# Kernel tuning notes

Hardware: AMD Instinct MI355X
Metric: run time of the kernel (lower is better)

The kernel has to match this reference:

```python
import jax, jax.numpy as jnp
import numpy as np

N, IN_DIM, HID = 8192, 128, 64
LEAKY_SLOPE = 0.2
MASK_VAL = -9e15


def lstm_step(x, W_ih, W_hh, b_ih, b_hh, h0, c0):
    # PyTorch LSTM single time step, gate order i, f, g, o
    gates = x @ W_ih.T + b_ih + h0 @ W_hh.T + b_hh
    i, f, g, o = jnp.split(gates, 4, axis=-1)
    c = jax.nn.sigmoid(f) * c0 + jax.nn.sigmoid(i) * jnp.tanh(g)
    h = jax.nn.sigmoid(o) * jnp.tanh(c)
    return h, c


def setup_inputs() -> dict:
    key = jax.random.key(0)
    ks = jax.random.split(key, 10)
    sc = 0.05
    x = jax.random.normal(ks[0], (N, IN_DIM), jnp.float32)
    adj = jax.random.randint(ks[1], (N, N), 0, 2).astype(jnp.float32)
    fea_W = jax.random.normal(ks[2], (IN_DIM, HID), jnp.float32) * sc
    fea_b = jnp.zeros((HID,), jnp.float32)
    gat_W = jax.random.normal(ks[3], (HID, IN_DIM), jnp.float32) * sc
    gat_a = jax.random.normal(ks[4], (2 * IN_DIM,), jnp.float32) * sc
    enc_W_ih = jax.random.normal(ks[5], (4 * HID, IN_DIM), jnp.float32) * sc
    enc_W_hh = jax.random.normal(ks[6], (4 * HID, HID), jnp.float32) * sc
    enc_b_ih = jnp.zeros((4 * HID,), jnp.float32)
    enc_b_hh = jnp.zeros((4 * HID,), jnp.float32)
    dec_W_ih = jax.random.normal(ks[7], (4 * IN_DIM, HID), jnp.float32) * sc
    dec_W_hh = jax.random.normal(ks[8], (4 * IN_DIM, IN_DIM), jnp.float32) * sc
    dec_b_ih = jnp.zeros((4 * IN_DIM,), jnp.float32)
    dec_b_hh = jnp.zeros((4 * IN_DIM,), jnp.float32)
    return dict(x=x, adj=adj, fea_W=fea_W, fea_b=fea_b, gat_W=gat_W, gat_a=gat_a,
                enc_W_ih=enc_W_ih, enc_W_hh=enc_W_hh, enc_b_ih=enc_b_ih, enc_b_hh=enc_b_hh,
                dec_W_ih=dec_W_ih, dec_W_hh=dec_W_hh, dec_b_ih=dec_b_ih, dec_b_hh=dec_b_hh)


def reference(x, adj, fea_W, fea_b, gat_W, gat_a,
              enc_W_ih, enc_W_hh, enc_b_ih, enc_b_hh,
              dec_W_ih, dec_W_hh, dec_b_ih, dec_b_hh):
    # structure branch: Linear + ReLU then GAT layer
    structure = jax.nn.relu(x @ fea_W + fea_b)            # [N, HID]
    Wh = structure @ gat_W                                # [N, IN_DIM]
    a1, a2 = gat_a[:IN_DIM], gat_a[IN_DIM:]
    e = jax.nn.leaky_relu((Wh @ a1)[:, None] + (Wh @ a2)[None, :], LEAKY_SLOPE)  # [N, N]
    scores = jnp.where(adj > 0, e, MASK_VAL)
    att = jax.nn.softmax(scores, axis=1)
    emb = jax.nn.elu(att @ Wh)                            # [N, IN_DIM]
    # attribute branch: seq_len=1 encoder/decoder LSTM with zero init states
    h0e = jnp.zeros((N, HID), x.dtype)
    h_enc, _ = lstm_step(x, enc_W_ih, enc_W_hh, enc_b_ih, enc_b_hh, h0e, h0e)
    h0d = jnp.zeros((N, IN_DIM), x.dtype)
    att_adj, _ = lstm_step(h_enc, dec_W_ih, dec_W_hh, dec_b_ih, dec_b_hh, h0d, h0d)  # [N, IN_DIM]
    con_adj = emb @ emb.T                                 # [N, N]
    return con_adj, att_adj
```

## Files before the change

### kernel.cpp

```cpp
#include <hip/hip_runtime.h>
#include <hip/hip_bf16.h>

typedef __hip_bfloat16 bf16_t;
typedef short bf16x8 __attribute__((ext_vector_type(8)));
typedef float f32x4 __attribute__((ext_vector_type(4)));

#define NROW 8192
#define LEAKY 0.2f

__device__ __forceinline__ float b2f(bf16_t v){ return __bfloat162float(v); }
__device__ __forceinline__ unsigned short f2b(float f){
  union { bf16_t h; unsigned short u; } cv; cv.h = __float2bfloat16(f); return cv.u;
}
__device__ __forceinline__ float sigf(float v){ return 1.0f / (1.0f + __expf(-v)); }

__global__ void k_probe(const unsigned short* __restrict__ x_raw, int* __restrict__ flag)
{
  const int lane = threadIdx.x;
  int cnt = 0;
  for (int k = lane; k < 512; k += 64){
    const int e = (x_raw[k] >> 7) & 0xff;
    cnt += (e >= 120 && e <= 130) ? 1 : 0;
  }
  #pragma unroll
  for (int s = 1; s < 64; s <<= 1) cnt += __shfl_xor(cnt, s, 64);
  if (lane == 0) flag[0] = (cnt < 384) ? 1 : 0;
}

__global__ __launch_bounds__(256) void k_cvt(
    const void* __restrict__ encW, const void* __restrict__ decW,
    const int* __restrict__ flag,
    unsigned short* __restrict__ encWb, unsigned short* __restrict__ decWb)
{
  const int idx = blockIdx.x*256 + threadIdx.x;
  const int isf32 = flag[0];
  if (idx < 32768){
    float v = isf32 ? ((const float*)encW)[idx] : b2f(((const bf16_t*)encW)[idx]);
    encWb[idx] = f2b(v);
  } else {
    const int j = idx - 32768;
    float v = isf32 ? ((const float*)decW)[j] : b2f(((const bf16_t*)decW)[j]);
    decWb[j] = f2b(v);
  }
}

__global__ __launch_bounds__(256) void k_feamask(
    const void* __restrict__ x, const void* __restrict__ adj,
    const void* __restrict__ fea_W, const void* __restrict__ fea_b,
    const void* __restrict__ gat_W, const void* __restrict__ gat_a,
    const int* __restrict__ flag,
    unsigned short* __restrict__ Whb_p, float* __restrict__ s1, float* __restrict__ s2,
    unsigned short* __restrict__ xb, unsigned char* __restrict__ mask8)
{
  const int r = blockIdx.x, tid = threadIdx.x;
  const int isf32 = flag[0];

  float4 mv0, mv1, mv2, mv3, mv4, mv5, mv6, mv7;
  bf16x8 bv0, bv1, bv2, bv3;
  if (isf32){
    const float4* arow = (const float4*)((const float*)adj + (size_t)r*NROW);
    mv0 = arow[(size_t)tid*2];         mv1 = arow[(size_t)tid*2+1];
    mv2 = arow[(size_t)(tid+256)*2];   mv3 = arow[(size_t)(tid+256)*2+1];
    mv4 = arow[(size_t)(tid+512)*2];   mv5 = arow[(size_t)(tid+512)*2+1];
    mv6 = arow[(size_t)(tid+768)*2];   mv7 = arow[(size_t)(tid+768)*2+1];
  } else {
    const unsigned short* arow = (const unsigned short*)adj + (size_t)r*NROW;
    bv0 = *(const bf16x8*)(arow + (size_t)tid*8);
    bv1 = *(const bf16x8*)(arow + (size_t)(tid+256)*8);
    bv2 = *(const bf16x8*)(arow + (size_t)(tid+512)*8);
    bv3 = *(const bf16x8*)(arow + (size_t)(tid+768)*8);
  }

  if (tid < 64){
    const int l = tid;
    float x0, x1;
    if (isf32){
      const float* xr = (const float*)x + (size_t)r*128;
      x0 = xr[l]; x1 = xr[l+64];
    } else {
      const bf16_t* xr = (const bf16_t*)x + (size_t)r*128;
      x0 = b2f(xr[l]); x1 = b2f(xr[l+64]);
    }
    xb[(size_t)r*128 + l]      = f2b(x0);
    xb[(size_t)r*128 + 64 + l] = f2b(x1);

    float acc = isf32 ? ((const float*)fea_b)[l] : b2f(((const bf16_t*)fea_b)[l]);
    if (isf32){
      const float* W = (const float*)fea_W;
      #pragma unroll
      for (int d=0; d<64; ++d) acc = fmaf(__shfl(x0, d, 64), W[d*64+l], acc);
      #pragma unroll
      for (int d=0; d<64; ++d) acc = fmaf(__shfl(x1, d, 64), W[(d+64)*64+l], acc);
    } else {
      const bf16_t* W = (const bf16_t*)fea_W;
      #pragma unroll
      for (int d=0; d<64; ++d) acc = fmaf(__shfl(x0, d, 64), b2f(W[d*64+l]), acc);
      #pragma unroll
      for (int d=0; d<64; ++d) acc = fmaf(__shfl(x1, d, 64), b2f(W[(d+64)*64+l]), acc);
    }
    const float stv = fmaxf(acc, 0.0f);

    float w0 = 0.f, w1 = 0.f;
    if (isf32){
      const float* W = (const float*)gat_W;
      #pragma unroll
      for (int d=0; d<64; ++d){
        const float sd = __shfl(stv, d, 64);
        w0 = fmaf(sd, W[d*128+l],    w0);
        w1 = fmaf(sd, W[d*128+64+l], w1);
      }
    } else {
      const bf16_t* W = (const bf16_t*)gat_W;
      #pragma unroll
      for (int d=0; d<64; ++d){
        const float sd = __shfl(stv, d, 64);
        w0 = fmaf(sd, b2f(W[d*128+l]),    w0);
        w1 = fmaf(sd, b2f(W[d*128+64+l]), w1);
      }
    }

    const size_t pbase = (size_t)(r >> 3)*1024 + (r & 7);
    Whb_p[pbase + (size_t)l*8]      = f2b(w0);
    Whb_p[pbase + (size_t)(l+64)*8] = f2b(w1);

    float a10, a11, a20, a21;
    if (isf32){
      const float* A = (const float*)gat_a;
      a10 = A[l]; a11 = A[l+64]; a20 = A[128+l]; a21 = A[192+l];
    } else {
      const bf16_t* A = (const bf16_t*)gat_a;
      a10 = b2f(A[l]); a11 = b2f(A[l+64]); a20 = b2f(A[128+l]); a21 = b2f(A[192+l]);
    }
    float r1 = w0*a10 + w1*a11;
    float r2 = w0*a20 + w1*a21;
    #pragma unroll
    for (int s=1; s<64; s<<=1){ r1 += __shfl_xor(r1, s, 64); r2 += __shfl_xor(r2, s, 64); }
    if (l == 0){ s1[r] = r1; s2[r] = r2; }
  }

  if (isf32){
    const float4 va[8] = { mv0, mv1, mv2, mv3, mv4, mv5, mv6, mv7 };
    #pragma unroll
    for (int k=0;k<4;++k){
      const float4 v0 = va[2*k], v1 = va[2*k+1];
      unsigned int m =
          (unsigned int)(v0.x>0.f)      | ((unsigned int)(v0.y>0.f)<<1) |
          ((unsigned int)(v0.z>0.f)<<2) | ((unsigned int)(v0.w>0.f)<<3) |
          ((unsigned int)(v1.x>0.f)<<4) | ((unsigned int)(v1.y>0.f)<<5) |
          ((unsigned int)(v1.z>0.f)<<6) | ((unsigned int)(v1.w>0.f)<<7);
      mask8[(size_t)r*1024 + tid + k*256] = (unsigned char)m;
    }
  } else {
    const bf16x8 vb[4] = { bv0, bv1, bv2, bv3 };
    #pragma unroll
    for (int k=0;k<4;++k){
      unsigned int m = 0;
      #pragma unroll
      for (int j=0;j<8;++j){
        union { short s; unsigned short u; } cv; cv.s = vb[k][j];
        union { unsigned short u; bf16_t h; } cv2; cv2.u = cv.u;
        m |= ((unsigned int)(b2f(cv2.h) > 0.f)) << j;
      }
      mask8[(size_t)r*1024 + tid + k*256] = (unsigned char)m;
    }
  }
}

__global__ __launch_bounds__(256) void k_enc2(
    const unsigned short* __restrict__ xb, const unsigned short* __restrict__ Wb,
    const void* __restrict__ b_ih, const void* __restrict__ b_hh,
    const int* __restrict__ flag, unsigned short* __restrict__ h_enc_b)
{
  __shared__ float g_lds[32][257];
  const int tid = threadIdx.x, lane = tid & 63, wv = tid >> 6;
  const int quad = lane >> 4, nn = lane & 15;
  const int rowbase = blockIdx.x * 32;
  const int rows_off = (wv & 1) * 16;
  const int col_off  = (wv >> 1) * 128;

  f32x4 acc[8];
  #pragma unroll
  for (int t=0;t<8;++t) acc[t] = (f32x4){0.f,0.f,0.f,0.f};

  #pragma unroll
  for (int ks=0; ks<4; ++ks){
    const int kb = ks*32 + quad*8;
    bf16x8 afrag = *(const bf16x8*)(xb + (size_t)(rowbase + rows_off + nn)*128 + kb);
    #pragma unroll
    for (int t=0;t<8;++t){
      bf16x8 bfrag = *(const bf16x8*)(Wb + (size_t)(col_off + t*16 + nn)*128 + kb);
      acc[t] = __builtin_amdgcn_mfma_f32_16x16x32_bf16(afrag, bfrag, acc[t], 0, 0, 0);
    }
  }
  #pragma unroll
  for (int t=0;t<8;++t)
    #pragma unroll
    for (int r=0;r<4;++r)
      g_lds[rows_off + quad*4 + r][col_off + t*16 + nn] = acc[t][r];
  __syncthreads();

  const int isf32 = flag[0];
  #pragma unroll
  for (int k=0;k<8;++k){
    const int idx = tid + k*256;
    const int r = idx >> 6, hid = idx & 63;
    float bi, bg, bo;
    if (isf32){
      const float* bi1 = (const float*)b_ih; const float* bi2 = (const float*)b_hh;
      bi = bi1[hid]     + bi2[hid];
      bg = bi1[128+hid] + bi2[128+hid];
      bo = bi1[192+hid] + bi2[192+hid];
    } else {
      const bf16_t* bi1 = (const bf16_t*)b_ih; const bf16_t* bi2 = (const bf16_t*)b_hh;
      bi = b2f(bi1[hid])     + b2f(bi2[hid]);
      bg = b2f(bi1[128+hid]) + b2f(bi2[128+hid]);
      bo = b2f(bi1[192+hid]) + b2f(bi2[192+hid]);
    }
    const float gi = g_lds[r][hid]     + bi;
    const float gg = g_lds[r][128+hid] + bg;
    const float go = g_lds[r][192+hid] + bo;
    const float c = tanhf(gg) * sigf(gi);
    const float h = tanhf(c)  * sigf(go);
    h_enc_b[(size_t)(rowbase + r)*64 + hid] = f2b(h);
  }
}

__global__ __launch_bounds__(256) void k_dec2(
    const unsigned short* __restrict__ hb, const unsigned short* __restrict__ Wb,
    const void* __restrict__ b_ih, const void* __restrict__ b_hh,
    const int* __restrict__ flag, void* __restrict__ d_out)
{
  __shared__ float g_lds[16][517];
  const int tid = threadIdx.x, lane = tid & 63, wv = tid >> 6;
  const int quad = lane >> 4, nn = lane & 15;
  const int rowbase = blockIdx.x * 16;
  const int col_off = wv * 128;

  f32x4 acc[8];
  #pragma unroll
  for (int t=0;t<8;++t) acc[t] = (f32x4){0.f,0.f,0.f,0.f};

  #pragma unroll
  for (int ks=0; ks<2; ++ks){
    const int kb = ks*32 + quad*8;
    bf16x8 afrag = *(const bf16x8*)(hb + (size_t)(rowbase + nn)*64 + kb);
    #pragma unroll
    for (int t=0;t<8;++t){
      bf16x8 bfrag = *(const bf16x8*)(Wb + (size_t)(col_off + t*16 + nn)*64 + kb);
      acc[t] = __builtin_amdgcn_mfma_f32_16x16x32_bf16(afrag, bfrag, acc[t], 0, 0, 0);
    }
  }
  #pragma unroll
  for (int t=0;t<8;++t)
    #pragma unroll
    for (int r=0;r<4;++r)
      g_lds[quad*4 + r][col_off + t*16 + nn] = acc[t][r];
  __syncthreads();

  const int isf32 = flag[0];
  #pragma unroll
  for (int k=0;k<8;++k){
    const int idx = tid + k*256;
    const int r = idx >> 7, col = idx & 127;
    float bi, bg, bo;
    if (isf32){
      const float* b1 = (const float*)b_ih; const float* b2 = (const float*)b_hh;
      bi = b1[col]     + b2[col];
      bg = b1[256+col] + b2[256+col];
      bo = b1[384+col] + b2[384+col];
    } else {
      const bf16_t* b1 = (const bf16_t*)b_ih; const bf16_t* b2v = (const bf16_t*)b_hh;
      bi = b2f(b1[col])     + b2f(b2v[col]);
      bg = b2f(b1[256+col]) + b2f(b2v[256+col]);
      bo = b2f(b1[384+col]) + b2f(b2v[384+col]);
    }
    const float gi = g_lds[r][col]     + bi;
    const float gg = g_lds[r][256+col] + bg;
    const float go = g_lds[r][384+col] + bo;
    const float c = tanhf(gg) * sigf(gi);
    const float h = tanhf(c)  * sigf(go);
    const size_t oidx = (size_t)NROW*NROW + (size_t)(rowbase + r)*128 + col;
    if (isf32) ((float*)d_out)[oidx] = h;
    else       ((unsigned short*)d_out)[oidx] = f2b(h);
  }
}

__global__ __launch_bounds__(512) void k_attn32s(
    const unsigned char* __restrict__ mask8, const unsigned short* __restrict__ Whb_p,
    const float* __restrict__ s1g, const float* __restrict__ s2g,
    float* __restrict__ Cpart, float* __restrict__ dnpart)
{
  __shared__ float C_lds[8][16*128];
  __shared__ float dn_lds[8][32];
  const int tid  = threadIdx.x;
  const int lane = tid & 63;
  const int wv   = tid >> 6;
  const int quad = lane >> 4;
  const int mrow = lane & 15;
  const int rowtile = blockIdx.x & 255;
  const int half    = blockIdx.x >> 8;
  const int rowbase = rowtile * 32;
  const float s1r0 = s1g[rowbase + mrow];
  const float s1r1 = s1g[rowbase + 16 + mrow];
  const unsigned char* mp0 = mask8 + (size_t)(rowbase + mrow) * 1024;
  const unsigned char* mp1 = mask8 + (size_t)(rowbase + 16 + mrow) * 1024;

  f32x4 acc[2][8];
  #pragma unroll
  for (int g=0;g<2;++g)
    #pragma unroll
    for (int t=0;t<8;++t) acc[g][t] = (f32x4){0.f,0.f,0.f,0.f};
  float dn0 = 0.f, dn1 = 0.f;

  const int jbeg = half*4096 + wv*512;
  for (int j0 = jbeg; j0 < jbeg + 512; j0 += 128){
    uint4 mw0 = *(const uint4*)(mp0 + (j0 >> 3));
    uint4 mw1 = *(const uint4*)(mp1 + (j0 >> 3));
    #pragma unroll
    for (int t4=0; t4<4; ++t4){
      const unsigned int mb0 = ((((const unsigned int*)&mw0)[t4]) >> (8*quad)) & 0xffu;
      const unsigned int mb1 = ((((const unsigned int*)&mw1)[t4]) >> (8*quad)) & 0xffu;
      const int kb = j0 + t4*32 + quad*8;
      float4 s2a = *(const float4*)(s2g + kb);
      float4 s2b = *(const float4*)(s2g + kb + 4);
      const float sv[8] = { s2a.x, s2a.y, s2a.z, s2a.w, s2b.x, s2b.y, s2b.z, s2b.w };
      bf16x8 af0, af1;
      #pragma unroll
      for (int b=0;b<8;++b){
        float v0 = s1r0 + sv[b];
        v0 = (v0 > 0.f) ? v0 : LEAKY * v0;
        const float e0 = __expf(v0);
        const float p0 = (mb0 & (1u<<b)) ? e0 : 0.f;
        dn0 += p0;
        af0[b] = (short)f2b(p0);
        float v1 = s1r1 + sv[b];
        v1 = (v1 > 0.f) ? v1 : LEAKY * v1;
        const float e1 = __expf(v1);
        const float p1 = (mb1 & (1u<<b)) ? e1 : 0.f;
        dn1 += p1;
        af1[b] = (short)f2b(p1);
      }
      const unsigned short* wb = Whb_p + (size_t)(kb >> 3)*1024 + mrow*8;
      #pragma unroll
      for (int t=0;t<8;++t){
        bf16x8 bfrag = *(const bf16x8*)(wb + t*128);
        acc[0][t] = __builtin_amdgcn_mfma_f32_16x16x32_bf16(af0, bfrag, acc[0][t], 0, 0, 0);
        acc[1][t] = __builtin_amdgcn_mfma_f32_16x16x32_bf16(af1, bfrag, acc[1][t], 0, 0, 0);
      }
    }
  }

  dn0 += __shfl_xor(dn0, 16, 64);
  dn0 += __shfl_xor(dn0, 32, 64);
  dn1 += __shfl_xor(dn1, 16, 64);
  dn1 += __shfl_xor(dn1, 32, 64);
  if (lane < 16){ dn_lds[wv][lane] = dn0; dn_lds[wv][16 + lane] = dn1; }

  float* Ch = Cpart + (size_t)half * NROW * 128;
  #pragma unroll
  for (int rg=0; rg<2; ++rg){
    #pragma unroll
    for (int t=0;t<8;++t){
      #pragma unroll
      for (int r=0;r<4;++r)
        C_lds[wv][(quad*4+r)*128 + t*16 + mrow] = acc[rg][t][r];
    }
    __syncthreads();
    for (int idx = tid; idx < 16*128; idx += 512){
      const int m = idx >> 7;
      const int d = idx & 127;
      const float v = C_lds[0][idx] + C_lds[1][idx] + C_lds[2][idx] + C_lds[3][idx]
                    + C_lds[4][idx] + C_lds[5][idx] + C_lds[6][idx] + C_lds[7][idx];
      Ch[(size_t)(rowbase + rg*16 + m)*128 + d] = v;
      if (d == 0){
        const float den = dn_lds[0][rg*16+m] + dn_lds[1][rg*16+m] + dn_lds[2][rg*16+m]
                        + dn_lds[3][rg*16+m] + dn_lds[4][rg*16+m] + dn_lds[5][rg*16+m]
                        + dn_lds[6][rg*16+m] + dn_lds[7][rg*16+m];
        dnpart[half*NROW + rowbase + rg*16 + m] = den;
      }
    }
    __syncthreads();
  }
}

__global__ __launch_bounds__(256) void k_merge(
    const float* __restrict__ Cpart, const float* __restrict__ dnpart,
    unsigned short* __restrict__ emb_p)
{
  const int tid = threadIdx.x;
  const int rowbase = blockIdx.x * 16;
  const float* C0 = Cpart;
  const float* C1 = Cpart + (size_t)NROW * 128;
  #pragma unroll
  for (int k=0;k<8;++k){
    const int idx = tid + k*256;
    const int m = idx >> 7;
    const int d = idx & 127;
    const int row = rowbase + m;
    const float den = dnpart[row] + dnpart[NROW + row];
    float v = (C0[(size_t)row*128 + d] + C1[(size_t)row*128 + d]) / den;
    v = (v > 0.f) ? v : (__expf(v) - 1.f);
    emb_p[(size_t)(d >> 3)*65536 + (size_t)row*8 + (d & 7)] = f2b(v);
  }
}

__global__ __launch_bounds__(256) void k_out(
    const unsigned short* __restrict__ emb_p, const int* __restrict__ flag,
    void* __restrict__ d_out)
{
  const int tid  = threadIdx.x;
  const int lane = tid & 63, wv = tid >> 6;
  const int quad = lane >> 4, nn = lane & 15;
  const int i0 = blockIdx.y * 128 + wv * 32;
  const int j0 = blockIdx.x * 64;

  f32x4 acc[2][4];
  #pragma unroll
  for (int a=0;a<2;++a)
    #pragma unroll
    for (int b=0;b<4;++b) acc[a][b] = (f32x4){0.f,0.f,0.f,0.f};

  #pragma unroll
  for (int ks=0; ks<4; ++ks){
    const int kb = ks*32 + quad*8;
    const unsigned short* base = emb_p + (size_t)(kb >> 3)*65536;
    bf16x8 a0 = *(const bf16x8*)(base + (size_t)(i0 + nn)*8);
    bf16x8 a1 = *(const bf16x8*)(base + (size_t)(i0 + 16 + nn)*8);
    #pragma unroll
    for (int t=0;t<4;++t){
      bf16x8 b = *(const bf16x8*)(base + (size_t)(j0 + t*16 + nn)*8);
      acc[0][t] = __builtin_amdgcn_mfma_f32_16x16x32_bf16(a0, b, acc[0][t], 0, 0, 0);
      acc[1][t] = __builtin_amdgcn_mfma_f32_16x16x32_bf16(a1, b, acc[1][t], 0, 0, 0);
    }
  }

  const int isf32 = flag[0];
  if (isf32){
    float* out = (float*)d_out;
    #pragma unroll
    for (int mi=0; mi<2; ++mi)
      #pragma unroll
      for (int t=0;t<4;++t)
        #pragma unroll
        for (int r=0;r<4;++r)
          out[(size_t)(i0 + mi*16 + quad*4 + r)*NROW + j0 + t*16 + nn] = acc[mi][t][r];
  } else {
    unsigned short* out = (unsigned short*)d_out;
    #pragma unroll
    for (int mi=0; mi<2; ++mi)
      #pragma unroll
      for (int t=0;t<4;++t)
        #pragma unroll
        for (int r=0;r<4;++r)
          out[(size_t)(i0 + mi*16 + quad*4 + r)*NROW + j0 + t*16 + nn] = f2b(acc[mi][t][r]);
  }
}

extern "C" void kernel_launch(void* const* d_in, const int* in_sizes, int n_in,
                              void* d_out, int out_size, void* d_ws, size_t ws_size,
                              hipStream_t stream)
{
  (void)in_sizes; (void)n_in; (void)out_size; (void)ws_size;
  const void* x        = d_in[0];
  const void* adj      = d_in[1];
  const void* fea_W    = d_in[2];
  const void* fea_b    = d_in[3];
  const void* gat_W    = d_in[4];
  const void* gat_a    = d_in[5];
  const void* enc_W_ih = d_in[6];
  const void* enc_b_ih = d_in[8];
  const void* enc_b_hh = d_in[9];
  const void* dec_W_ih = d_in[10];
  const void* dec_b_ih = d_in[12];
  const void* dec_b_hh = d_in[13];

  char* ws = (char*)d_ws;
  unsigned short* Whb_p   = (unsigned short*)ws;
  unsigned short* emb_p   = (unsigned short*)(ws + (2u<<20));
  unsigned short* xb      = (unsigned short*)(ws + (4u<<20));
  unsigned short* h_enc_b = (unsigned short*)(ws + (6u<<20));
  unsigned char*  mask8   = (unsigned char*) (ws + (7u<<20));
  float* s1    = (float*)(ws + (15u<<20));
  float* s2    = (float*)(ws + (15u<<20) + 32768);
  unsigned short* encWb = (unsigned short*)(ws + (15u<<20) + 65536);
  unsigned short* decWb = (unsigned short*)(ws + (15u<<20) + 65536 + 65536);
  int* flag = (int*)(ws + (15u<<20) + 3*65536);
  float* Cpart  = (float*)(ws + (16u<<20));
  float* dnpart = (float*)(ws + (24u<<20));

  k_probe<<<1, 64, 0, stream>>>((const unsigned short*)x, flag);
  k_cvt<<<256, 256, 0, stream>>>(enc_W_ih, dec_W_ih, flag, encWb, decWb);
  k_feamask<<<NROW, 256, 0, stream>>>(x, adj, fea_W, fea_b, gat_W, gat_a, flag,
                                      Whb_p, s1, s2, xb, mask8);
  k_enc2<<<256, 256, 0, stream>>>(xb, encWb, enc_b_ih, enc_b_hh, flag, h_enc_b);
  k_dec2<<<512, 256, 0, stream>>>(h_enc_b, decWb, dec_b_ih, dec_b_hh, flag, d_out);
  k_attn32s<<<512, 512, 0, stream>>>(mask8, Whb_p, s1, s2, Cpart, dnpart);
  k_merge<<<512, 256, 0, stream>>>(Cpart, dnpart, emb_p);
  k_out<<<dim3(128, 64), 256, 0, stream>>>(emb_p, flag, d_out);
}
```

Before: 569.6 us.

## Process one adjacency row per wave in feature/mask kernel with staged loads

The feature/mask kernel now assigns one row per wavefront (four rows per block) instead of one row per 256-thread block. Previously only one wave did the small feature matmul while three idled. Now every wave does both the feature projection and the mask packing for its own row. The adjacency row reads are split into four stages so loads overlap with packing, and the bf16 mask test uses integer comparisons. This raises per-wave register use and serial work per wave in exchange for better lane utilization.

```diff
diff --git a/kernel.cpp b/kernel.cpp
--- a/kernel.cpp
+++ b/kernel.cpp
@@ -13,6 +13,23 @@
   union { bf16_t h; unsigned short u; } cv; cv.h = __float2bfloat16(f); return cv.u;
 }
 __device__ __forceinline__ float sigf(float v){ return 1.0f / (1.0f + __expf(-v)); }
+
+__device__ __forceinline__ unsigned char packf(float4 v0, float4 v1){
+  return (unsigned char)(
+      (unsigned int)(v0.x>0.f)      | ((unsigned int)(v0.y>0.f)<<1) |
+      ((unsigned int)(v0.z>0.f)<<2) | ((unsigned int)(v0.w>0.f)<<3) |
+      ((unsigned int)(v1.x>0.f)<<4) | ((unsigned int)(v1.y>0.f)<<5) |
+      ((unsigned int)(v1.z>0.f)<<6) | ((unsigned int)(v1.w>0.f)<<7));
+}
+__device__ __forceinline__ unsigned char packb(bf16x8 v){
+  unsigned int m = 0;
+  #pragma unroll
+  for (int j=0;j<8;++j){
+    union { short s; unsigned short u; } cv; cv.s = v[j];
+    m |= ((unsigned int)(cv.u > 0 && cv.u < 0x8000)) << j;
+  }
+  return (unsigned char)m;
+}
 
 __global__ void k_probe(const unsigned short* __restrict__ x_raw, int* __restrict__ flag)
 {
@@ -44,7 +61,7 @@
   }
 }
 
-__global__ __launch_bounds__(256) void k_feamask(
+__global__ __launch_bounds__(256) void k_feamask4(
     const void* __restrict__ x, const void* __restrict__ adj,
     const void* __restrict__ fea_W, const void* __restrict__ fea_b,
     const void* __restrict__ gat_W, const void* __restrict__ gat_a,
@@ -52,37 +69,51 @@
     unsigned short* __restrict__ Whb_p, float* __restrict__ s1, float* __restrict__ s2,
     unsigned short* __restrict__ xb, unsigned char* __restrict__ mask8)
 {
-  const int r = blockIdx.x, tid = threadIdx.x;
+  const int tid = threadIdx.x;
+  const int wv  = tid >> 6;
+  const int l   = tid & 63;
+  const int row = blockIdx.x * 4 + wv;
   const int isf32 = flag[0];
 
-  float4 mv0, mv1, mv2, mv3, mv4, mv5, mv6, mv7;
-  bf16x8 bv0, bv1, bv2, bv3;
+  unsigned char* mrow = mask8 + (size_t)row * 1024;
+
+  float4 vA0,vA1,vA2,vA3, vB0,vB1,vB2,vB3;
+  float4 wA0,wA1,wA2,wA3, wB0,wB1,wB2,wB3;
+  bf16x8 q0,q1,q2,q3, p0,p1,p2,p3;
+  const float4* a4 = (const float4*)((const float*)adj + (size_t)row*NROW);
+  const unsigned short* a2 = (const unsigned short*)adj + (size_t)row*NROW;
+
   if (isf32){
-    const float4* arow = (const float4*)((const float*)adj + (size_t)r*NROW);
-    mv0 = arow[(size_t)tid*2];         mv1 = arow[(size_t)tid*2+1];
-    mv2 = arow[(size_t)(tid+256)*2];   mv3 = arow[(size_t)(tid+256)*2+1];
-    mv4 = arow[(size_t)(tid+512)*2];   mv5 = arow[(size_t)(tid+512)*2+1];
-    mv6 = arow[(size_t)(tid+768)*2];   mv7 = arow[(size_t)(tid+768)*2+1];
+    vA0 = a4[(size_t)((0*4+0)*64 + l)*2]; vB0 = a4[(size_t)((0*4+0)*64 + l)*2 + 1];
+    vA1 = a4[(size_t)((0*4+1)*64 + l)*2]; vB1 = a4[(size_t)((0*4+1)*64 + l)*2 + 1];
+    vA2 = a4[(size_t)((0*4+2)*64 + l)*2]; vB2 = a4[(size_t)((0*4+2)*64 + l)*2 + 1];
+    vA3 = a4[(size_t)((0*4+3)*64 + l)*2]; vB3 = a4[(size_t)((0*4+3)*64 + l)*2 + 1];
+    wA0 = a4[(size_t)((1*4+0)*64 + l)*2]; wB0 = a4[(size_t)((1*4+0)*64 + l)*2 + 1];
+    wA1 = a4[(size_t)((1*4+1)*64 + l)*2]; wB1 = a4[(size_t)((1*4+1)*64 + l)*2 + 1];
+    wA2 = a4[(size_t)((1*4+2)*64 + l)*2]; wB2 = a4[(size_t)((1*4+2)*64 + l)*2 + 1];
+    wA3 = a4[(size_t)((1*4+3)*64 + l)*2]; wB3 = a4[(size_t)((1*4+3)*64 + l)*2 + 1];
   } else {
-    const unsigned short* arow = (const unsigned short*)adj + (size_t)r*NROW;
-    bv0 = *(const bf16x8*)(arow + (size_t)tid*8);
-    bv1 = *(const bf16x8*)(arow + (size_t)(tid+256)*8);
-    bv2 = *(const bf16x8*)(arow + (size_t)(tid+512)*8);
-    bv3 = *(const bf16x8*)(arow + (size_t)(tid+768)*8);
-  }
-
-  if (tid < 64){
-    const int l = tid;
+    q0 = *(const bf16x8*)(a2 + (size_t)((0*4+0)*64 + l)*8);
+    q1 = *(const bf16x8*)(a2 + (size_t)((0*4+1)*64 + l)*8);
+    q2 = *(const bf16x8*)(a2 + (size_t)((0*4+2)*64 + l)*8);
+    q3 = *(const bf16x8*)(a2 + (size_t)((0*4+3)*64 + l)*8);
+    p0 = *(const bf16x8*)(a2 + (size_t)((1*4+0)*64 + l)*8);
+    p1 = *(const bf16x8*)(a2 + (size_t)((1*4+1)*64 + l)*8);
+    p2 = *(const bf16x8*)(a2 + (size_t)((1*4+2)*64 + l)*8);
+    p3 = *(const bf16x8*)(a2 + (size_t)((1*4+3)*64 + l)*8);
+  }
+
+  {
     float x0, x1;
     if (isf32){
-      const float* xr = (const float*)x + (size_t)r*128;
+      const float* xr = (const float*)x + (size_t)row*128;
       x0 = xr[l]; x1 = xr[l+64];
     } else {
-      const bf16_t* xr = (const bf16_t*)x + (size_t)r*128;
+      const bf16_t* xr = (const bf16_t*)x + (size_t)row*128;
       x0 = b2f(xr[l]); x1 = b2f(xr[l+64]);
     }
-    xb[(size_t)r*128 + l]      = f2b(x0);
-    xb[(size_t)r*128 + 64 + l] = f2b(x1);
+    xb[(size_t)row*128 + l]      = f2b(x0);
+    xb[(size_t)row*128 + 64 + l] = f2b(x1);
 
     float acc = isf32 ? ((const float*)fea_b)[l] : b2f(((const bf16_t*)fea_b)[l]);
     if (isf32){
@@ -119,7 +150,7 @@
       }
     }
 
-    const size_t pbase = (size_t)(r >> 3)*1024 + (r & 7);
+    const size_t pbase = (size_t)(row >> 3)*1024 + (row & 7);
     Whb_p[pbase + (size_t)l*8]      = f2b(w0);
     Whb_p[pbase + (size_t)(l+64)*8] = f2b(w1);
 
@@ -135,34 +166,59 @@
     float r2 = w0*a20 + w1*a21;
     #pragma unroll
     for (int s=1; s<64; s<<=1){ r1 += __shfl_xor(r1, s, 64); r2 += __shfl_xor(r2, s, 64); }
-    if (l == 0){ s1[r] = r1; s2[r] = r2; }
+    if (l == 0){ s1[row] = r1; s2[row] = r2; }
   }
 
   if (isf32){
-    const float4 va[8] = { mv0, mv1, mv2, mv3, mv4, mv5, mv6, mv7 };
-    #pragma unroll
-    for (int k=0;k<4;++k){
-      const float4 v0 = va[2*k], v1 = va[2*k+1];
-      unsigned int m =
-          (unsigned int)(v0.x>0.f)      | ((unsigned int)(v0.y>0.f)<<1) |
-          ((unsigned int)(v0.z>0.f)<<2) | ((unsigned int)(v0.w>0.f)<<3) |
-          ((unsigned int)(v1.x>0.f)<<4) | ((unsigned int)(v1.y>0.f)<<5) |
-          ((unsigned int)(v1.z>0.f)<<6) | ((unsigned int)(v1.w>0.f)<<7);
-      mask8[(size_t)r*1024 + tid + k*256] = (unsigned char)m;
-    }
+    mrow[(0*4+0)*64 + l] = packf(vA0, vB0);
+    mrow[(0*4+1)*64 + l] = packf(vA1, vB1);
+    mrow[(0*4+2)*64 + l] = packf(vA2, vB2);
+    mrow[(0*4+3)*64 + l] = packf(vA3, vB3);
+    vA0 = a4[(size_t)((2*4+0)*64 + l)*2]; vB0 = a4[(size_t)((2*4+0)*64 + l)*2 + 1];
+    vA1 = a4[(size_t)((2*4+1)*64 + l)*2]; vB1 = a4[(size_t)((2*4+1)*64 + l)*2 + 1];
+    vA2 = a4[(size_t)((2*4+2)*64 + l)*2]; vB2 = a4[(size_t)((2*4+2)*64 + l)*2 + 1];
+    vA3 = a4[(size_t)((2*4+3)*64 + l)*2]; vB3 = a4[(size_t)((2*4+3)*64 + l)*2 + 1];
+    mrow[(1*4+0)*64 + l] = packf(wA0, wB0);
+    mrow[(1*4+1)*64 + l] = packf(wA1, wB1);
+    mrow[(1*4+2)*64 + l] = packf(wA2, wB2);
+    mrow[(1*4+3)*64 + l] = packf(wA3, wB3);
+    wA0 = a4[(size_t)((3*4+0)*64 + l)*2]; wB0 = a4[(size_t)((3*4+0)*64 + l)*2 + 1];
+    wA1 = a4[(size_t)((3*4+1)*64 + l)*2]; wB1 = a4[(size_t)((3*4+1)*64 + l)*2 + 1];
+    wA2 = a4[(size_t)((3*4+2)*64 + l)*2]; wB2 = a4[(size_t)((3*4+2)*64 + l)*2 + 1];
+    wA3 = a4[(size_t)((3*4+3)*64 + l)*2]; wB3 = a4[(size_t)((3*4+3)*64 + l)*2 + 1];
+    mrow[(2*4+0)*64 + l] = packf(vA0, vB0);
+    mrow[(2*4+1)*64 + l] = packf(vA1, vB1);
+    mrow[(2*4+2)*64 + l] = packf(vA2, vB2);
+    mrow[(2*4+3)*64 + l] = packf(vA3, vB3);
+    mrow[(3*4+0)*64 + l] = packf(wA0, wB0);
+    mrow[(3*4+1)*64 + l] = packf(wA1, wB1);
+    mrow[(3*4+2)*64 + l] = packf(wA2, wB2);
+    mrow[(3*4+3)*64 + l] = packf(wA3, wB3);
   } else {
-    const bf16x8 vb[4] = { bv0, bv1, bv2, bv3 };
-    #pragma unroll
-    for (int k=0;k<4;++k){
-      unsigned int m = 0;
-      #pragma unroll
-      for (int j=0;j<8;++j){
-        union { short s; unsigned short u; } cv; cv.s = vb[k][j];
-        union { unsigned short u; bf16_t h; } cv2; cv2.u = cv.u;
-        m |= ((unsigned int)(b2f(cv2.h) > 0.f)) << j;
-      }
-      mask8[(size_t)r*1024 + tid + k*256] = (unsigned char)m;
-    }
+    mrow[(0*4+0)*64 + l] = packb(q0);
+    mrow[(0*4+1)*64 + l] = packb(q1);
+    mrow[(0*4+2)*64 + l] = packb(q2);
+    mrow[(0*4+3)*64 + l] = packb(q3);
+    q0 = *(const bf16x8*)(a2 + (size_t)((2*4+0)*64 + l)*8);
+    q1 = *(const bf16x8*)(a2 + (size_t)((2*4+1)*64 + l)*8);
+    q2 = *(const bf16x8*)(a2 + (size_t)((2*4+2)*64 + l)*8);
+    q3 = *(const bf16x8*)(a2 + (size_t)((2*4+3)*64 + l)*8);
+    mrow[(1*4+0)*64 + l] = packb(p0);
+    mrow[(1*4+1)*64 + l] = packb(p1);
+    mrow[(1*4+2)*64 + l] = packb(p2);
+    mrow[(1*4+3)*64 + l] = packb(p3);
+    p0 = *(const bf16x8*)(a2 + (size_t)((3*4+0)*64 + l)*8);
+    p1 = *(const bf16x8*)(a2 + (size_t)((3*4+1)*64 + l)*8);
+    p2 = *(const bf16x8*)(a2 + (size_t)((3*4+2)*64 + l)*8);
+    p3 = *(const bf16x8*)(a2 + (size_t)((3*4+3)*64 + l)*8);
+    mrow[(2*4+0)*64 + l] = packb(q0);
+    mrow[(2*4+1)*64 + l] = packb(q1);
+    mrow[(2*4+2)*64 + l] = packb(q2);
+    mrow[(2*4+3)*64 + l] = packb(q3);
+    mrow[(3*4+0)*64 + l] = packb(p0);
+    mrow[(3*4+1)*64 + l] = packb(p1);
+    mrow[(3*4+2)*64 + l] = packb(p2);
+    mrow[(3*4+3)*64 + l] = packb(p3);
   }
 }
 
@@ -490,8 +546,8 @@
 
   k_probe<<<1, 64, 0, stream>>>((const unsigned short*)x, flag);
   k_cvt<<<256, 256, 0, stream>>>(enc_W_ih, dec_W_ih, flag, encWb, decWb);
-  k_feamask<<<NROW, 256, 0, stream>>>(x, adj, fea_W, fea_b, gat_W, gat_a, flag,
-                                      Whb_p, s1, s2, xb, mask8);
+  k_feamask4<<<2048, 256, 0, stream>>>(x, adj, fea_W, fea_b, gat_W, gat_a, flag,
+                                       Whb_p, s1, s2, xb, mask8);
   k_enc2<<<256, 256, 0, stream>>>(xb, encWb, enc_b_ih, enc_b_hh, flag, h_enc_b);
   k_dec2<<<512, 256, 0, stream>>>(h_enc_b, decWb, dec_b_ih, dec_b_hh, flag, d_out);
   k_attn32s<<<512, 512, 0, stream>>>(mask8, Whb_p, s1, s2, Cpart, dnpart);
```

New measurement: 658.4 us. 1.16x slower.
